# Kernel optimization log

Hardware: AMD Instinct MI355X
Metric: run time of the kernel (lower is better)

## Reference

```python
import jax, jax.numpy as jnp
import numpy as np
import math

EMBED_DIM = 2048
NUM_HEADS = 32
GROUPS = 4
HEAD_DIM = EMBED_DIM // NUM_HEADS  # 64
HPG = NUM_HEADS // GROUPS          # heads per group = 8


def setup_inputs() -> dict:
    key = jax.random.key(0)
    k_x, k_wq, k_bq, k_wkv, k_bkv = jax.random.split(key, 5)
    B, L = 4, 4096
    scale = 1.0 / math.sqrt(EMBED_DIM)
    return {
        "x": jax.random.normal(k_x, (B, L, EMBED_DIM), dtype=jnp.float32),
        "Wq": jax.random.normal(k_wq, (EMBED_DIM, EMBED_DIM), dtype=jnp.float32) * scale,
        "bq": jax.random.normal(k_bq, (EMBED_DIM,), dtype=jnp.float32) * 0.01,
        "Wkv": jax.random.normal(k_wkv, (EMBED_DIM, 2 * HEAD_DIM * GROUPS), dtype=jnp.float32) * scale,
        "bkv": jax.random.normal(k_bkv, (2 * HEAD_DIM * GROUPS,), dtype=jnp.float32) * 0.01,
    }


def reference(x, Wq, bq, Wkv, bkv):
    B, L, _ = x.shape
    # projections
    q = (x @ Wq + bq).reshape(B, L, GROUPS, HPG, HEAD_DIM)          # blghd
    kv = (x @ Wkv + bkv).reshape(B, L, GROUPS, 2, HEAD_DIM)
    k, v = kv[:, :, :, 0], kv[:, :, :, 1]                            # blgd
    # scores: q @ k^T with k of shape (..., 1, head_dim) -> (..., HPG, 1)
    scores = jnp.einsum("blghd,blgd->blgh", q, k)[..., None] / math.sqrt(HEAD_DIM)
    attn = jax.nn.softmax(scores, axis=-1)                           # size-1 axis -> ones
    # attn @ v: (..., HPG, 1) @ (..., 1, head_dim) -> (..., HPG, head_dim)
    out = attn * v[:, :, :, None, :]                                 # blghd
    return out.reshape(B, L, EMBED_DIM)
```

## Files before the change

kernel.cpp:

```cpp
#include <hip/hip_runtime.h>


#define EMBED 2048
#define BK 64
#define KIT (EMBED / BK)
#define SA 72
#define SV 68

typedef _Float16 half8 __attribute__((ext_vector_type(8)));
typedef _Float16 half4v __attribute__((ext_vector_type(4)));
typedef float f32x4 __attribute__((ext_vector_type(4)));

#define BAR() asm volatile("s_waitcnt lgkmcnt(0)\ns_barrier" ::: "memory")

__global__ __launch_bounds__(256) void prep_b(const float* __restrict__ Wkv,
                                              _Float16* __restrict__ Bt) {
  const int t = threadIdx.x;
  const int kb = blockIdx.x * 4;
  const int vcol = ((t >> 6) * 128) + 64 + (t & 63);
  float v[4];
#pragma unroll
  for (int i = 0; i < 4; ++i) v[i] = Wkv[(size_t)(kb + i) * 512 + vcol];
  half4v h;
#pragma unroll
  for (int i = 0; i < 4; ++i) h[i] = (_Float16)v[i];
  *(half4v*)&Bt[(size_t)t * EMBED + kb] = h;
}

__global__ __launch_bounds__(256, 8) void gqa_main(
    const float* __restrict__ x, const _Float16* __restrict__ Bt,
    const float* __restrict__ bkv, float* __restrict__ out) {
  __shared__ __align__(16) char smem[(32 + 64) * SA * 2];
  _Float16* As = (_Float16*)smem;
  _Float16* Bs = As + 32 * SA;
  float* Vs = (float*)smem;

  const int tid = threadIdx.x;
  const int wave = tid >> 6;
  const int lane = tid & 63;
  const int lm = lane & 15;
  const int lq = lane >> 4;
  const int bi = blockIdx.x;
  const int nb = (bi >> 3) & 3;
  const int mb = ((bi >> 5) << 3) | (bi & 7);
  const int mi2 = wave & 1;
  const int ni2 = wave >> 1;

  const int ar = tid >> 3, ac = (tid & 7) * 8;
  const float* ap = x + (size_t)(mb * 32 + ar) * EMBED + ac;
  _Float16* aw = As + ar * SA + ac;
  const int br = tid >> 2, bc = (tid & 3) * 16;
  const _Float16* bp = Bt + (size_t)(nb * 64 + br) * EMBED + bc;
  _Float16* bw = Bs + br * SA + bc;

  const _Float16* ard = As + (mi2 * 16 + lm) * SA + lq * 8;
  const _Float16* brd = Bs + (ni2 * 32 + lm) * SA + lq * 8;

  f32x4 pa0[2], pa1[2];
  half8 pb0[2], pb1[2];

#define LOADAB(kt, PA, PB)                       \
  {                                              \
    const float* p_ = ap + (kt) * BK;            \
    PA[0] = *(const f32x4*)p_;                   \
    PA[1] = *(const f32x4*)(p_ + 4);             \
    const _Float16* q_ = bp + (kt) * BK;         \
    PB[0] = *(const half8*)q_;                   \
    PB[1] = *(const half8*)(q_ + 8);             \
  }
#define STAGE(PA, PB)                            \
  {                                              \
    half8 h_;                                    \
    _Pragma("unroll") for (int j_ = 0; j_ < 4; ++j_) \
        h_[j_] = (_Float16)PA[0][j_];            \
    _Pragma("unroll") for (int j_ = 0; j_ < 4; ++j_) \
        h_[4 + j_] = (_Float16)PA[1][j_];        \
    *(half8*)aw = h_;                            \
    *(half8*)bw = PB[0];                         \
    *(half8*)(bw + 8) = PB[1];                   \
  }
#define COMPUTE()                                                         \
  {                                                                       \
    half8 af_[2], bf_[2][2];                                              \
    _Pragma("unroll") for (int ks_ = 0; ks_ < 2; ++ks_)                   \
        af_[ks_] = *(const half8*)(ard + ks_ * 32);                       \
    _Pragma("unroll") for (int ni_ = 0; ni_ < 2; ++ni_)                   \
        _Pragma("unroll") for (int ks_ = 0; ks_ < 2; ++ks_)               \
            bf_[ni_][ks_] = *(const half8*)(brd + ni_ * 16 * SA + ks_ * 32); \
    _Pragma("unroll") for (int ni_ = 0; ni_ < 2; ++ni_)                   \
        _Pragma("unroll") for (int ks_ = 0; ks_ < 2; ++ks_)               \
            acc[ni_] = __builtin_amdgcn_mfma_f32_16x16x32_f16(            \
                af_[ks_], bf_[ni_][ks_], acc[ni_], 0, 0, 0);              \
  }

  f32x4 acc[2] = {};

  LOADAB(0, pa0, pb0);
  LOADAB(1, pa1, pb1);

  for (int kt = 0; kt < KIT; kt += 2) {
    STAGE(pa0, pb0);
    BAR();
    if (kt + 2 < KIT) LOADAB(kt + 2, pa0, pb0);
    COMPUTE();
    BAR();
    STAGE(pa1, pb1);
    BAR();
    if (kt + 3 < KIT) LOADAB(kt + 3, pa1, pb1);
    COMPUTE();
    BAR();
  }

#pragma unroll
  for (int ni = 0; ni < 2; ++ni) {
    const int nc = ni2 * 32 + ni * 16 + lm;
    const float bias = bkv[nb * 128 + 64 + nc];
    f32x4 v = acc[ni];
#pragma unroll
    for (int r = 0; r < 4; ++r) {
      Vs[(mi2 * 16 + lq * 4 + r) * SV + nc] = v[r] + bias;
    }
  }
  BAR();

  f32x4* out4 = (f32x4*)(out + (size_t)(mb * 32) * EMBED + nb * 512);
#pragma unroll 8
  for (int i = 0; i < 16; ++i) {
    const int f = i * 256 + tid;
    const int row = f >> 7;
    const int c4 = f & 127;
    const int d4 = c4 & 15;
    out4[(size_t)row * 512 + c4] = *(const f32x4*)&Vs[row * SV + d4 * 4];
  }
}

extern "C" void kernel_launch(void* const* d_in, const int* in_sizes, int n_in,
                              void* d_out, int out_size, void* d_ws, size_t ws_size,
                              hipStream_t stream) {
  const float* x = (const float*)d_in[0];
  const float* Wkv = (const float*)d_in[3];
  const float* bkv = (const float*)d_in[4];
  float* out = (float*)d_out;
  _Float16* Bt = (_Float16*)d_ws;

  prep_b<<<512, 256, 0, stream>>>(Wkv, Bt);
  gqa_main<<<2048, 256, 0, stream>>>(x, Bt, bkv, out);
}
```

Baseline: 308.9 us.

## Load MFMA operands directly from global memory, one block per 16 rows

Removes the LDS staging of the A (x) and B (V weight) tiles, along with the barriers. Each wave now reads its MFMA fragments straight from global memory, double-buffered in registers. Each block covers 16 rows and all four groups, so every x row is read from DRAM once instead of four times, and the grid shrinks to 1024 blocks. The cost is that LDS reuse is gone, so each wave loads its own B fragments and the four waves re-read the same x fragments. Occupancy is also capped lower through launch bounds.

```diff
diff --git a/kernel.cpp b/kernel.cpp
--- a/kernel.cpp
+++ b/kernel.cpp
@@ -2,16 +2,11 @@
 
 
 #define EMBED 2048
-#define BK 64
-#define KIT (EMBED / BK)
-#define SA 72
-#define SV 68
+#define SV 272
 
 typedef _Float16 half8 __attribute__((ext_vector_type(8)));
 typedef _Float16 half4v __attribute__((ext_vector_type(4)));
 typedef float f32x4 __attribute__((ext_vector_type(4)));
-
-#define BAR() asm volatile("s_waitcnt lgkmcnt(0)\ns_barrier" ::: "memory")
 
 __global__ __launch_bounds__(256) void prep_b(const float* __restrict__ Wkv,
                                               _Float16* __restrict__ Bt) {
@@ -27,110 +22,80 @@
   *(half4v*)&Bt[(size_t)t * EMBED + kb] = h;
 }
 
-__global__ __launch_bounds__(256, 8) void gqa_main(
+__global__ __launch_bounds__(256, 4) void gqa_main(
     const float* __restrict__ x, const _Float16* __restrict__ Bt,
     const float* __restrict__ bkv, float* __restrict__ out) {
-  __shared__ __align__(16) char smem[(32 + 64) * SA * 2];
-  _Float16* As = (_Float16*)smem;
-  _Float16* Bs = As + 32 * SA;
-  float* Vs = (float*)smem;
+  __shared__ __align__(16) float Vs[16][SV];
 
   const int tid = threadIdx.x;
-  const int wave = tid >> 6;
+  const int w = tid >> 6;
   const int lane = tid & 63;
   const int lm = lane & 15;
   const int lq = lane >> 4;
-  const int bi = blockIdx.x;
-  const int nb = (bi >> 3) & 3;
-  const int mb = ((bi >> 5) << 3) | (bi & 7);
-  const int mi2 = wave & 1;
-  const int ni2 = wave >> 1;
+  const int row0 = blockIdx.x * 16;
 
-  const int ar = tid >> 3, ac = (tid & 7) * 8;
-  const float* ap = x + (size_t)(mb * 32 + ar) * EMBED + ac;
-  _Float16* aw = As + ar * SA + ac;
-  const int br = tid >> 2, bc = (tid & 3) * 16;
-  const _Float16* bp = Bt + (size_t)(nb * 64 + br) * EMBED + bc;
-  _Float16* bw = Bs + br * SA + bc;
+  const float* apx = x + (size_t)(row0 + lm) * EMBED + lq * 8;
+  const _Float16* bp0 = Bt + (size_t)(w * 64 + lm) * EMBED + lq * 8;
 
-  const _Float16* ard = As + (mi2 * 16 + lm) * SA + lq * 8;
-  const _Float16* brd = Bs + (ni2 * 32 + lm) * SA + lq * 8;
+  f32x4 a0_0, a1_0, a0_1, a1_1;
+  half8 b_0[4], b_1[4];
 
-  f32x4 pa0[2], pa1[2];
-  half8 pb0[2], pb1[2];
-
-#define LOADAB(kt, PA, PB)                       \
-  {                                              \
-    const float* p_ = ap + (kt) * BK;            \
-    PA[0] = *(const f32x4*)p_;                   \
-    PA[1] = *(const f32x4*)(p_ + 4);             \
-    const _Float16* q_ = bp + (kt) * BK;         \
-    PB[0] = *(const half8*)q_;                   \
-    PB[1] = *(const half8*)(q_ + 8);             \
+#define LOADX(h, A0, A1, B)                          \
+  {                                                  \
+    const float* p_ = apx + (h) * 32;                \
+    A0 = *(const f32x4*)p_;                          \
+    A1 = *(const f32x4*)(p_ + 4);                    \
+    const _Float16* q_ = bp0 + (h) * 32;             \
+    B[0] = *(const half8*)q_;                        \
+    B[1] = *(const half8*)(q_ + 16 * EMBED);         \
+    B[2] = *(const half8*)(q_ + 32 * EMBED);         \
+    B[3] = *(const half8*)(q_ + 48 * EMBED);         \
   }
-#define STAGE(PA, PB)                            \
-  {                                              \
-    half8 h_;                                    \
-    _Pragma("unroll") for (int j_ = 0; j_ < 4; ++j_) \
-        h_[j_] = (_Float16)PA[0][j_];            \
-    _Pragma("unroll") for (int j_ = 0; j_ < 4; ++j_) \
-        h_[4 + j_] = (_Float16)PA[1][j_];        \
-    *(half8*)aw = h_;                            \
-    *(half8*)bw = PB[0];                         \
-    *(half8*)(bw + 8) = PB[1];                   \
-  }
-#define COMPUTE()                                                         \
-  {                                                                       \
-    half8 af_[2], bf_[2][2];                                              \
-    _Pragma("unroll") for (int ks_ = 0; ks_ < 2; ++ks_)                   \
-        af_[ks_] = *(const half8*)(ard + ks_ * 32);                       \
-    _Pragma("unroll") for (int ni_ = 0; ni_ < 2; ++ni_)                   \
-        _Pragma("unroll") for (int ks_ = 0; ks_ < 2; ++ks_)               \
-            bf_[ni_][ks_] = *(const half8*)(brd + ni_ * 16 * SA + ks_ * 32); \
-    _Pragma("unroll") for (int ni_ = 0; ni_ < 2; ++ni_)                   \
-        _Pragma("unroll") for (int ks_ = 0; ks_ < 2; ++ks_)               \
-            acc[ni_] = __builtin_amdgcn_mfma_f32_16x16x32_f16(            \
-                af_[ks_], bf_[ni_][ks_], acc[ni_], 0, 0, 0);              \
+#define CONS(A0, A1, B)                                                  \
+  {                                                                      \
+    half8 af_;                                                           \
+    _Pragma("unroll") for (int j_ = 0; j_ < 4; ++j_)                     \
+        af_[j_] = (_Float16)A0[j_];                                      \
+    _Pragma("unroll") for (int j_ = 0; j_ < 4; ++j_)                     \
+        af_[4 + j_] = (_Float16)A1[j_];                                  \
+    _Pragma("unroll") for (int n_ = 0; n_ < 4; ++n_)                     \
+        acc[n_] = __builtin_amdgcn_mfma_f32_16x16x32_f16(af_, B[n_],     \
+                                                         acc[n_], 0, 0, 0); \
   }
 
-  f32x4 acc[2] = {};
+  f32x4 acc[4] = {};
 
-  LOADAB(0, pa0, pb0);
-  LOADAB(1, pa1, pb1);
+  LOADX(0, a0_0, a1_0, b_0);
+  LOADX(1, a0_1, a1_1, b_1);
 
-  for (int kt = 0; kt < KIT; kt += 2) {
-    STAGE(pa0, pb0);
-    BAR();
-    if (kt + 2 < KIT) LOADAB(kt + 2, pa0, pb0);
-    COMPUTE();
-    BAR();
-    STAGE(pa1, pb1);
-    BAR();
-    if (kt + 3 < KIT) LOADAB(kt + 3, pa1, pb1);
-    COMPUTE();
-    BAR();
+  for (int h = 0; h < 64; h += 2) {
+    CONS(a0_0, a1_0, b_0);
+    if (h + 2 < 64) LOADX(h + 2, a0_0, a1_0, b_0);
+    CONS(a0_1, a1_1, b_1);
+    if (h + 3 < 64) LOADX(h + 3, a0_1, a1_1, b_1);
   }
 
 #pragma unroll
-  for (int ni = 0; ni < 2; ++ni) {
-    const int nc = ni2 * 32 + ni * 16 + lm;
-    const float bias = bkv[nb * 128 + 64 + nc];
+  for (int ni = 0; ni < 4; ++ni) {
+    const int n = w * 64 + ni * 16 + lm;
+    const float bias = bkv[w * 128 + 64 + ni * 16 + lm];
     f32x4 v = acc[ni];
 #pragma unroll
     for (int r = 0; r < 4; ++r) {
-      Vs[(mi2 * 16 + lq * 4 + r) * SV + nc] = v[r] + bias;
+      Vs[lq * 4 + r][n] = v[r] + bias;
     }
   }
-  BAR();
+  __syncthreads();
 
-  f32x4* out4 = (f32x4*)(out + (size_t)(mb * 32) * EMBED + nb * 512);
+  f32x4* out4 = (f32x4*)(out + (size_t)row0 * EMBED);
 #pragma unroll 8
-  for (int i = 0; i < 16; ++i) {
+  for (int i = 0; i < 32; ++i) {
     const int f = i * 256 + tid;
-    const int row = f >> 7;
-    const int c4 = f & 127;
+    const int row = f >> 9;
+    const int c4 = f & 511;
+    const int grp = c4 >> 7;
     const int d4 = c4 & 15;
-    out4[(size_t)row * 512 + c4] = *(const f32x4*)&Vs[row * SV + d4 * 4];
+    out4[(size_t)row * 512 + c4] = *(const f32x4*)&Vs[row][grp * 64 + d4 * 4];
   }
 }
 
@@ -144,5 +109,5 @@
   _Float16* Bt = (_Float16*)d_ws;
 
   prep_b<<<512, 256, 0, stream>>>(Wkv, Bt);
-  gqa_main<<<2048, 256, 0, stream>>>(x, Bt, bkv, out);
+  gqa_main<<<1024, 256, 0, stream>>>(x, Bt, bkv, out);
 }
```

Result: slower. 398.6 us (+29.0%).
